# Performance work log

Measured on AMD Instinct MI355X. Metric: run time of the kernel, lower is better.

Reference implementation:

```python
import jax, jax.numpy as jnp
import numpy as np

B, T, IN, HID, OUT, NB = 64, 150, 120, 1024, 35, 8
VTH = 1.0


def _branch_mask(rng, out_dim, in_size):
    # For each output neuron: a random permutation of inputs split into NB equal branches.
    perm = np.argsort(rng.random((out_dim, in_size)), axis=1)          # [out, in]
    branch = (np.arange(in_size) * NB) // in_size                      # branch id of each slot
    rows = (np.arange(out_dim)[:, None] * NB + branch[None, :]).ravel()
    m = np.zeros((out_dim * NB, in_size), dtype=np.bool_)
    m[rows, perm.ravel()] = True
    return jnp.asarray(m)


def setup_inputs() -> dict:
    rng = np.random.default_rng(0)

    def lin(o, i):
        bound = 1.0 / np.sqrt(i)
        w = rng.uniform(-bound, bound, (o, i)).astype(np.float32)
        b = rng.uniform(-bound, bound, (o,)).astype(np.float32)
        return jnp.asarray(w), jnp.asarray(b)

    def tau(*shape):
        return jnp.asarray(rng.uniform(0.0, 4.0, shape).astype(np.float32))

    w1, b1 = lin(HID * NB, IN)
    w2, b2 = lin(HID * NB, HID)
    w3, b3 = lin(HID * NB, HID)
    wr, br = lin(OUT, HID)

    x = jax.random.normal(jax.random.key(0), (B, 1, T, IN), dtype=jnp.float32)

    return dict(
        x=x,
        w1=w1, b1=b1, tau_m1=tau(HID), tau_n1=tau(HID, NB),
        w2=w2, b2=b2, tau_m2=tau(HID), tau_n2=tau(HID, NB),
        w3=w3, b3=b3, tau_m3=tau(HID), tau_n3=tau(HID, NB),
        wr=wr, br=br, tau_mr=tau(OUT),
        mask1=_branch_mask(rng, HID, IN),
        mask2=_branch_mask(rng, HID, HID),
        mask3=_branch_mask(rng, HID, HID),
    )


@jax.custom_vjp
def act_fun(x):  # spike with rectangular surrogate gradient
    return (x > 0.0).astype(x.dtype)

def _act_fwd(x):
    return act_fun(x), x

def _act_bwd(x, g):
    return (g * (jnp.abs(x) < 0.5).astype(g.dtype),)

act_fun.defvjp(_act_fwd, _act_bwd)


def _dh_step(spk_in, d, mem, spk, wm, b, tau_m, tau_n):
    # wm: pre-masked weight [HID*NB, D_in]
    dense = (spk_in @ wm.T + b).reshape(-1, HID, NB)      # [B, HID, NB]
    beta = jax.nn.sigmoid(tau_n)                          # [HID, NB]
    d = beta * d + (1.0 - beta) * dense                   # branch decay
    l_input = d.sum(axis=2)                               # [B, HID]
    alpha = jax.nn.sigmoid(tau_m)
    mem = mem * alpha + (1.0 - alpha) * l_input - VTH * spk  # soft reset (prev spike)
    spk = act_fun(mem - VTH)
    return d, mem, spk


def _forward(x, w1, b1, tau_m1, tau_n1, w2, b2, tau_m2, tau_n2,
             w3, b3, tau_m3, tau_n3, wr, br, tau_mr, mask1, mask2, mask3):
    b_sz = x.shape[0]
    wm1 = w1 * mask1.astype(w1.dtype)
    wm2 = w2 * mask2.astype(w2.dtype)
    wm3 = w3 * mask3.astype(w3.dtype)
    alpha_r = jax.nn.sigmoid(tau_mr)

    xt = x[:, 0].transpose(1, 0, 2)                        # [T, B, IN]

    z_bh = jnp.zeros((b_sz, HID), x.dtype)
    z_bhn = jnp.zeros((b_sz, HID, NB), x.dtype)
    carry0 = (z_bhn, z_bh, z_bh, z_bhn, z_bh, z_bh, z_bhn, z_bh, z_bh,
              jnp.zeros((b_sz, OUT), x.dtype), jnp.zeros((b_sz, OUT), x.dtype))

    def step(carry, inp_t):
        d1, m1, s1, d2, m2, s2, d3, m3, s3, mr, acc = carry
        d1, m1, s1 = _dh_step(inp_t, d1, m1, s1, wm1, b1, tau_m1, tau_n1)
        d2, m2, s2 = _dh_step(s1,    d2, m2, s2, wm2, b2, tau_m2, tau_n2)
        d3, m3, s3 = _dh_step(s2,    d3, m3, s3, wm3, b3, tau_m3, tau_n3)
        mr = mr * alpha_r + (1.0 - alpha_r) * (s3 @ wr.T + br)
        acc = acc + mr
        return (d1, m1, s1, d2, m2, s2, d3, m3, s3, mr, acc), None

    (_, _, _, _, _, _, _, _, _, _, acc), _ = jax.lax.scan(step, carry0, xt)
    return jax.nn.log_softmax(acc / xt.shape[0], axis=1)


def reference(x, w1, b1, tau_m1, tau_n1, w2, b2, tau_m2, tau_n2,
              w3, b3, tau_m3, tau_n3, wr, br, tau_mr, mask1, mask2, mask3):
    return _forward(x, w1, b1, tau_m1, tau_n1, w2, b2, tau_m2, tau_n2,
                    w3, b3, tau_m3, tau_n3, wr, br, tau_mr, mask1, mask2, mask3)
```

## Files before the change

### kernel.cpp

```cpp
#include <hip/hip_runtime.h>
#include <stdint.h>

#define BATCH 64
#define TT    150
#define INSZ  120
#define HID   1024
#define OUTN  35
#define NBR   8
#define TPAD  160
#define CH    8
#define NCHUNK 19

#define XT_OFF  0
#define S1_OFF  4608000
#define S2_OFF  5918720
#define S3_OFF  7229440
#define Y_OFF   8540160
#define ACC_OFF 9884160

__global__ __launch_bounds__(256) void k_tx(const float* __restrict__ x,
                                            float* __restrict__ xT) {
    const int t = blockIdx.x;
    __shared__ float tile[INSZ * 65];
    for (int e = threadIdx.x; e < INSZ * 64; e += 256) {
        const int b = e / INSZ, i = e - b * INSZ;
        tile[i * 65 + b] = x[((size_t)b * TT + t) * INSZ + i];
    }
    __syncthreads();
    for (int e = threadIdx.x; e < INSZ * 64; e += 256) {
        const int i = e >> 6, b = e & 63;
        xT[((size_t)t * INSZ + i) * 64 + b] = tile[i * 65 + b];
    }
}

template <int DIN, int NNZ, int MODE>
__global__ __launch_bounds__(512, 8) void k_layer(
    const float* __restrict__ w,
    const void* __restrict__ maskp,
    const float* __restrict__ bias,
    const float* __restrict__ tau_m,
    const float* __restrict__ tau_n,
    const float* __restrict__ xin,
    const uint64_t* __restrict__ inm,
    uint64_t* __restrict__ outm)
{
    const int tid  = threadIdx.x;
    const int lane = tid & 63;
    const int wid  = tid >> 6;
    const int h    = blockIdx.x;
    const int r    = h * NBR + wid;

    __shared__ uint2 ent[NBR * NNZ];
    __shared__ float red[2][NBR * CH * 64];

    inm = (const uint64_t*)__builtin_assume_aligned(inm, 64);

    const unsigned char* m8  = (const unsigned char*)maskp;
    const int*           m32 = (const int*)maskp;
    {
        const int base = wid * NNZ;
        int cnt = 0;
        for (int c = 0; c * 64 < DIN; ++c) {
            const int i = c * 64 + lane;
            int   mv = 0;
            float wv = 0.f;
            if (i < DIN) {
                mv = m8[(size_t)r * DIN + i];
                wv = w[(size_t)r * DIN + i];
            }
            const unsigned long long bal = __ballot(mv != 0);
            const int pos = __popcll(bal & ((1ull << lane) - 1ull));
            if (mv && cnt + pos < NNZ)
                ent[base + cnt + pos] = make_uint2(__float_as_uint(wv), (unsigned)i);
            cnt += __popcll(bal);
        }
        if (cnt != NNZ) {
            cnt = 0;
            for (int c = 0; c * 64 < DIN; ++c) {
                const int i = c * 64 + lane;
                int   mv = 0;
                float wv = 0.f;
                if (i < DIN) {
                    mv = m32[(size_t)r * DIN + i];
                    wv = w[(size_t)r * DIN + i];
                }
                const unsigned long long bal = __ballot(mv != 0);
                const int pos = __popcll(bal & ((1ull << lane) - 1ull));
                if (mv) ent[base + cnt + pos] =
                            make_uint2(__float_as_uint(wv), (unsigned)i);
                cnt += __popcll(bal);
            }
        }
    }
    __syncthreads();

    const float be = 1.f / (1.f + expf(-tau_n[r]));
    const float om = 1.f - be;
    const float bb = bias[r];
    const float al  = 1.f / (1.f + expf(-tau_m[h]));
    const float oma = 1.f - al;

    float d = 0.f, mem = 0.f, spkprev = 0.f;
    const int base = wid * NNZ;

    for (int tc = 0; tc < NCHUNK; ++tc) {
        const int t0  = tc * CH;
        const int buf = tc & 1;
        float a[CH];
#pragma unroll
        for (int k = 0; k < CH; ++k) a[k] = 0.f;

        if constexpr (MODE == 1) {
#pragma unroll 4
            for (int j = 0; j < NNZ; ++j) {
                const uint2 e  = ent[base + j];
                const int   ix = __builtin_amdgcn_readfirstlane((int)e.y);
                const float wv = __uint_as_float(e.x);
                const ulonglong4* p =
                    (const ulonglong4*)(inm + (size_t)ix * TPAD + t0);
                const ulonglong4 ma = p[0], mb = p[1];
                uint64_t m[CH] = {ma.x, ma.y, ma.z, ma.w,
                                  mb.x, mb.y, mb.z, mb.w};
#pragma unroll
                for (int k = 0; k < CH; ++k) {
                    float s;
                    asm("v_cndmask_b32 %0, 0, %1, %2"
                        : "=v"(s) : "v"(wv), "s"(m[k]));
                    a[k] += s;
                }
            }
        } else {
            const float* xb = xin + (size_t)t0 * DIN * 64;
#pragma unroll 3
            for (int j = 0; j < NNZ; ++j) {
                const uint2 e  = ent[base + j];
                const int   ix = __builtin_amdgcn_readfirstlane((int)e.y);
                const float wv = __uint_as_float(e.x);
#pragma unroll
                for (int k = 0; k < CH; ++k)
                    a[k] += wv * xb[((size_t)k * DIN + ix) * 64 + lane];
            }
        }

#pragma unroll
        for (int k = 0; k < CH; ++k) {
            d = be * d + om * (a[k] + bb);
            red[buf][(wid * CH + k) * 64 + lane] = d;
        }
        __syncthreads();

        if (wid == 0) {
#pragma unroll
            for (int k = 0; k < CH; ++k) {
                const float r0 = red[buf][(0 * CH + k) * 64 + lane];
                const float r1 = red[buf][(1 * CH + k) * 64 + lane];
                const float r2 = red[buf][(2 * CH + k) * 64 + lane];
                const float r3 = red[buf][(3 * CH + k) * 64 + lane];
                const float r4 = red[buf][(4 * CH + k) * 64 + lane];
                const float r5 = red[buf][(5 * CH + k) * 64 + lane];
                const float r6 = red[buf][(6 * CH + k) * 64 + lane];
                const float r7 = red[buf][(7 * CH + k) * 64 + lane];
                const float p01 = r0 + r1, p23 = r2 + r3;
                const float p45 = r4 + r5, p67 = r6 + r7;
                const float l = ((p01 + p23) + p45) + p67;
                if (t0 + k < TT) {
                    mem = al * mem + oma * l - spkprev;
                    spkprev = (mem > 1.0f) ? 1.f : 0.f;
                    const unsigned long long bal = __ballot(mem > 1.0f);
                    if (lane == 0) outm[(size_t)h * TPAD + (t0 + k)] = bal;
                }
            }
        }
    }
}

__global__ __launch_bounds__(256) void k_ry(const float* __restrict__ wr,
                                            const uint64_t* __restrict__ s3m,
                                            float* __restrict__ Y) {
    const int lane  = threadIdx.x & 63;
    const int wid   = __builtin_amdgcn_readfirstlane(threadIdx.x >> 6);
    const int o  = blockIdx.x / NCHUNK;
    const int t0 = (blockIdx.x % NCHUNK) * CH;
    s3m = (const uint64_t*)__builtin_assume_aligned(s3m, 64);
    const float* wrow = wr + (size_t)o * HID;
    __shared__ float red[4 * CH * 64];
    float acc[CH];
#pragma unroll
    for (int k = 0; k < CH; ++k) acc[k] = 0.f;
#pragma unroll 4
    for (int ii = 0; ii < HID / 4; ++ii) {
        const int i = wid * (HID / 4) + ii;
        const float wv = wrow[i];
        const ulonglong4* p =
            (const ulonglong4*)(s3m + (size_t)i * TPAD + t0);
        const ulonglong4 ma = p[0], mb = p[1];
        uint64_t m[CH] = {ma.x, ma.y, ma.z, ma.w, mb.x, mb.y, mb.z, mb.w};
#pragma unroll
        for (int k = 0; k < CH; ++k) {
            float s;
            asm("v_cndmask_b32 %0, 0, %1, %2" : "=v"(s) : "v"(wv), "s"(m[k]));
            acc[k] += s;
        }
    }
#pragma unroll
    for (int k = 0; k < CH; ++k)
        red[(wid * CH + k) * 64 + lane] = acc[k];
    __syncthreads();
    if (wid == 0) {
#pragma unroll
        for (int k = 0; k < CH; ++k) {
            if (t0 + k >= TT) break;
            const float v = ((red[(0 * CH + k) * 64 + lane]
                            + red[(1 * CH + k) * 64 + lane])
                            + red[(2 * CH + k) * 64 + lane])
                            + red[(3 * CH + k) * 64 + lane];
            Y[((size_t)(t0 + k) * OUTN + o) * 64 + lane] = v;
        }
    }
}

__global__ void k_racc(const float* __restrict__ Y,
                       const float* __restrict__ br,
                       const float* __restrict__ tau_mr,
                       float* __restrict__ ACC) {
    const int o = blockIdx.x, lane = threadIdx.x;
    const float ar  = 1.f / (1.f + expf(-tau_mr[o]));
    const float bro = br[o];
    float acc = 0.f, q = ar;
    for (int t = TT - 1; t >= 0; --t) {
        const float y = Y[((size_t)t * OUTN + o) * 64 + lane] + bro;
        acc += y * (1.f - q);
        q *= ar;
    }
    ACC[o * 64 + lane] = acc;
}

__global__ void k_smax(const float* __restrict__ ACC, float* __restrict__ out) {
    const int b = threadIdx.x;
    float v[OUTN];
    float mx = -3.4e38f;
    for (int o = 0; o < OUTN; ++o) {
        v[o] = ACC[o * 64 + b] / (float)TT;
        mx = fmaxf(mx, v[o]);
    }
    float sum = 0.f;
    for (int o = 0; o < OUTN; ++o) sum += expf(v[o] - mx);
    const float lse = mx + logf(sum);
    for (int o = 0; o < OUTN; ++o) out[b * OUTN + o] = v[o] - lse;
}

extern "C" void kernel_launch(void* const* d_in, const int* in_sizes, int n_in,
                              void* d_out, int out_size, void* d_ws,
                              size_t ws_size, hipStream_t stream) {
    (void)in_sizes; (void)n_in; (void)out_size; (void)ws_size;
    const float* x   = (const float*)d_in[0];
    const float* w1  = (const float*)d_in[1];
    const float* b1  = (const float*)d_in[2];
    const float* tm1 = (const float*)d_in[3];
    const float* tn1 = (const float*)d_in[4];
    const float* w2  = (const float*)d_in[5];
    const float* b2  = (const float*)d_in[6];
    const float* tm2 = (const float*)d_in[7];
    const float* tn2 = (const float*)d_in[8];
    const float* w3  = (const float*)d_in[9];
    const float* b3  = (const float*)d_in[10];
    const float* tm3 = (const float*)d_in[11];
    const float* tn3 = (const float*)d_in[12];
    const float* wr  = (const float*)d_in[13];
    const float* br  = (const float*)d_in[14];
    const float* tmr = (const float*)d_in[15];
    const void*  m1  = d_in[16];
    const void*  m2  = d_in[17];
    const void*  m3  = d_in[18];
    float* out = (float*)d_out;

    char* ws = (char*)d_ws;
    float*    xT  = (float*)(ws + XT_OFF);
    uint64_t* s1m = (uint64_t*)(ws + S1_OFF);
    uint64_t* s2m = (uint64_t*)(ws + S2_OFF);
    uint64_t* s3m = (uint64_t*)(ws + S3_OFF);
    float*    Y   = (float*)(ws + Y_OFF);
    float*    ACC = (float*)(ws + ACC_OFF);

    k_tx<<<TT, 256, 0, stream>>>(x, xT);
    k_layer<INSZ, 15, 0><<<HID, 512, 0, stream>>>(
        w1, m1, b1, tm1, tn1, xT, nullptr, s1m);
    k_layer<HID, 128, 1><<<HID, 512, 0, stream>>>(
        w2, m2, b2, tm2, tn2, nullptr, s1m, s2m);
    k_layer<HID, 128, 1><<<HID, 512, 0, stream>>>(
        w3, m3, b3, tm3, tn3, nullptr, s2m, s3m);
    k_ry<<<OUTN * NCHUNK, 256, 0, stream>>>(wr, s3m, Y);
    k_racc<<<OUTN, 64, 0, stream>>>(Y, br, tmr, ACC);
    k_smax<<<1, 64, 0, stream>>>(ACC, out);
}
```

Before: 1.657 ms.

## Pre-pack sparse weights into compact global arrays and relayout input transpose

```diff
diff --git a/kernel.cpp b/kernel.cpp
--- a/kernel.cpp
+++ b/kernel.cpp
@@ -1,42 +1,79 @@
 #include <hip/hip_runtime.h>
 #include <stdint.h>
 
-#define BATCH 64
-#define TT    150
-#define INSZ  120
-#define HID   1024
-#define OUTN  35
-#define NBR   8
-#define TPAD  160
-#define CH    8
+#define TT     150
+#define INSZ   120
+#define HID    1024
+#define OUTN   35
+#define NBR    8
+#define TP     152
+#define CH     8
 #define NCHUNK 19
 
-#define XT_OFF  0
-#define S1_OFF  4608000
-#define S2_OFF  5918720
-#define S3_OFF  7229440
-#define Y_OFF   8540160
-#define ACC_OFF 9884160
-
-__global__ __launch_bounds__(256) void k_tx(const float* __restrict__ x,
-                                            float* __restrict__ xT) {
-    const int t = blockIdx.x;
-    __shared__ float tile[INSZ * 65];
-    for (int e = threadIdx.x; e < INSZ * 64; e += 256) {
-        const int b = e / INSZ, i = e - b * INSZ;
-        tile[i * 65 + b] = x[((size_t)b * TT + t) * INSZ + i];
-    }
-    __syncthreads();
-    for (int e = threadIdx.x; e < INSZ * 64; e += 256) {
-        const int i = e >> 6, b = e & 63;
-        xT[((size_t)t * INSZ + i) * 64 + b] = tile[i * 65 + b];
-    }
-}
-
-template <int DIN, int NNZ, int MODE>
+#define SA_OFF   0
+#define SB_OFF   1245184
+#define PK_OFF   2490368
+#define XT_OFF   3538944
+#define Y_OFF    2490368
+#define ACC_OFF  3866624
+
+template <int DIN, int NNZ_EXPECT, int NNZ_OUT, int RSTRIDE, int WOFF>
+__global__ __launch_bounds__(512) void k_pack(
+    const float* __restrict__ w, const void* __restrict__ maskp,
+    uint8_t* __restrict__ dst) {
+    const int lane = threadIdx.x & 63;
+    const int wid  = __builtin_amdgcn_readfirstlane(threadIdx.x >> 6);
+    const int r    = blockIdx.x * 8 + wid;
+    uint16_t* di = (uint16_t*)(dst + (size_t)r * RSTRIDE);
+    float*    dw = (float*)(dst + (size_t)r * RSTRIDE + WOFF);
+    const unsigned char* m8  = (const unsigned char*)maskp;
+    const int*           m32 = (const int*)maskp;
+
+    int cnt = 0;
+    for (int c = 0; c * 64 < DIN; ++c) {
+        const int i = c * 64 + lane;
+        int   mv = 0; float wv = 0.f;
+        if (i < DIN) { mv = m8[(size_t)r * DIN + i]; wv = w[(size_t)r * DIN + i]; }
+        const unsigned long long bal = __ballot(mv != 0);
+        const int pos = __popcll(bal & ((1ull << lane) - 1ull));
+        if (mv && cnt + pos < NNZ_OUT) { di[cnt + pos] = (uint16_t)i; dw[cnt + pos] = wv; }
+        cnt += __popcll(bal);
+    }
+    if (cnt != NNZ_EXPECT) {
+        cnt = 0;
+        for (int c = 0; c * 64 < DIN; ++c) {
+            const int i = c * 64 + lane;
+            int   mv = 0; float wv = 0.f;
+            if (i < DIN) { mv = m32[(size_t)r * DIN + i]; wv = w[(size_t)r * DIN + i]; }
+            const unsigned long long bal = __ballot(mv != 0);
+            const int pos = __popcll(bal & ((1ull << lane) - 1ull));
+            if (mv && cnt + pos < NNZ_OUT) { di[cnt + pos] = (uint16_t)i; dw[cnt + pos] = wv; }
+            cnt += __popcll(bal);
+        }
+    }
+    for (int f = cnt + lane; f < NNZ_OUT; f += 64) { di[f] = 0; dw[f] = 0.f; }
+}
+
+__global__ __launch_bounds__(256) void k_tx2(const float* __restrict__ x,
+                                             float* __restrict__ xT2) {
+    const int e = blockIdx.x * 256 + threadIdx.x;
+    const int c = e / 7680;
+    const int rem = e - c * 7680;
+    const int b = rem / INSZ, i = rem - b * INSZ;
+    float v[CH];
+#pragma unroll
+    for (int k = 0; k < CH; ++k) {
+        const int t = c * CH + k;
+        v[k] = (t < TT) ? x[((size_t)b * TT + t) * INSZ + i] : 0.f;
+    }
+    float* dst = xT2 + ((size_t)i * 64 + b) * TP + c * CH;
+    *(float4*)dst       = make_float4(v[0], v[1], v[2], v[3]);
+    *(float4*)(dst + 4) = make_float4(v[4], v[5], v[6], v[7]);
+}
+
+template <int DIN, int NNZ, int MODE, int RSTRIDE, int WOFF>
 __global__ __launch_bounds__(512, 8) void k_layer(
-    const float* __restrict__ w,
-    const void* __restrict__ maskp,
+    const uint8_t* __restrict__ pk,
     const float* __restrict__ bias,
     const float* __restrict__ tau_m,
     const float* __restrict__ tau_n,
@@ -44,55 +81,17 @@
     const uint64_t* __restrict__ inm,
     uint64_t* __restrict__ outm)
 {
-    const int tid  = threadIdx.x;
-    const int lane = tid & 63;
-    const int wid  = tid >> 6;
+    const int lane = threadIdx.x & 63;
+    const int wid  = __builtin_amdgcn_readfirstlane(threadIdx.x >> 6);
     const int h    = blockIdx.x;
     const int r    = h * NBR + wid;
 
-    __shared__ uint2 ent[NBR * NNZ];
     __shared__ float red[2][NBR * CH * 64];
 
+    const uint8_t*  pkrow = pk + (size_t)r * RSTRIDE;
+    const uint32_t* idxp  = (const uint32_t*)pkrow;
+    const float*    wp    = (const float*)(pkrow + WOFF);
     inm = (const uint64_t*)__builtin_assume_aligned(inm, 64);
-
-    const unsigned char* m8  = (const unsigned char*)maskp;
-    const int*           m32 = (const int*)maskp;
-    {
-        const int base = wid * NNZ;
-        int cnt = 0;
-        for (int c = 0; c * 64 < DIN; ++c) {
-            const int i = c * 64 + lane;
-            int   mv = 0;
-            float wv = 0.f;
-            if (i < DIN) {
-                mv = m8[(size_t)r * DIN + i];
-                wv = w[(size_t)r * DIN + i];
-            }
-            const unsigned long long bal = __ballot(mv != 0);
-            const int pos = __popcll(bal & ((1ull << lane) - 1ull));
-            if (mv && cnt + pos < NNZ)
-                ent[base + cnt + pos] = make_uint2(__float_as_uint(wv), (unsigned)i);
-            cnt += __popcll(bal);
-        }
-        if (cnt != NNZ) {
-            cnt = 0;
-            for (int c = 0; c * 64 < DIN; ++c) {
-                const int i = c * 64 + lane;
-                int   mv = 0;
-                float wv = 0.f;
-                if (i < DIN) {
-                    mv = m32[(size_t)r * DIN + i];
-                    wv = w[(size_t)r * DIN + i];
-                }
-                const unsigned long long bal = __ballot(mv != 0);
-                const int pos = __popcll(bal & ((1ull << lane) - 1ull));
-                if (mv) ent[base + cnt + pos] =
-                            make_uint2(__float_as_uint(wv), (unsigned)i);
-                cnt += __popcll(bal);
-            }
-        }
-    }
-    __syncthreads();
 
     const float be = 1.f / (1.f + expf(-tau_n[r]));
     const float om = 1.f - be;
@@ -101,7 +100,6 @@
     const float oma = 1.f - al;
 
     float d = 0.f, mem = 0.f, spkprev = 0.f;
-    const int base = wid * NNZ;
 
     for (int tc = 0; tc < NCHUNK; ++tc) {
         const int t0  = tc * CH;
@@ -111,34 +109,54 @@
         for (int k = 0; k < CH; ++k) a[k] = 0.f;
 
         if constexpr (MODE == 1) {
-#pragma unroll 4
-            for (int j = 0; j < NNZ; ++j) {
-                const uint2 e  = ent[base + j];
-                const int   ix = __builtin_amdgcn_readfirstlane((int)e.y);
-                const float wv = __uint_as_float(e.x);
-                const ulonglong4* p =
-                    (const ulonglong4*)(inm + (size_t)ix * TPAD + t0);
-                const ulonglong4 ma = p[0], mb = p[1];
-                uint64_t m[CH] = {ma.x, ma.y, ma.z, ma.w,
-                                  mb.x, mb.y, mb.z, mb.w};
+            for (int jj = 0; jj < NNZ / 2; ++jj) {
+                const uint32_t pair = idxp[jj];
+                const int ix0 = (int)(pair & 0xffffu);
+                const int ix1 = (int)(pair >> 16);
+                const float2 wpair = ((const float2*)wp)[jj];
+                const float w0 = wpair.x, w1 = wpair.y;
+                const ulonglong4* p0 =
+                    (const ulonglong4*)(inm + (size_t)ix0 * TP + t0);
+                const ulonglong4* p1 =
+                    (const ulonglong4*)(inm + (size_t)ix1 * TP + t0);
+                const ulonglong4 a0 = p0[0], b0 = p0[1];
+                const ulonglong4 a1 = p1[0], b1 = p1[1];
+                const uint64_t m0[CH] = {a0.x, a0.y, a0.z, a0.w,
+                                         b0.x, b0.y, b0.z, b0.w};
+                const uint64_t m1[CH] = {a1.x, a1.y, a1.z, a1.w,
+                                         b1.x, b1.y, b1.z, b1.w};
 #pragma unroll
                 for (int k = 0; k < CH; ++k) {
-                    float s;
+                    float s0, s1;
                     asm("v_cndmask_b32 %0, 0, %1, %2"
-                        : "=v"(s) : "v"(wv), "s"(m[k]));
-                    a[k] += s;
+                        : "=v"(s0) : "v"(w0), "s"(m0[k]));
+                    a[k] += s0;
+                    asm("v_cndmask_b32 %0, 0, %1, %2"
+                        : "=v"(s1) : "v"(w1), "s"(m1[k]));
+                    a[k] += s1;
                 }
             }
         } else {
-            const float* xb = xin + (size_t)t0 * DIN * 64;
-#pragma unroll 3
-            for (int j = 0; j < NNZ; ++j) {
-                const uint2 e  = ent[base + j];
-                const int   ix = __builtin_amdgcn_readfirstlane((int)e.y);
-                const float wv = __uint_as_float(e.x);
-#pragma unroll
-                for (int k = 0; k < CH; ++k)
-                    a[k] += wv * xb[((size_t)k * DIN + ix) * 64 + lane];
+            for (int jj = 0; jj < NNZ / 2; ++jj) {
+                const uint32_t pair = idxp[jj];
+                const int ix0 = (int)(pair & 0xffffu);
+                const int ix1 = (int)(pair >> 16);
+                const float2 wpair = ((const float2*)wp)[jj];
+                const float w0 = wpair.x, w1 = wpair.y;
+                const float* q0 = xin + (size_t)ix0 * (64 * TP) + lane * TP + t0;
+                const float* q1 = xin + (size_t)ix1 * (64 * TP) + lane * TP + t0;
+                const float4 xa0 = *(const float4*)q0;
+                const float4 xb0 = *(const float4*)(q0 + 4);
+                const float4 xa1 = *(const float4*)q1;
+                const float4 xb1 = *(const float4*)(q1 + 4);
+                a[0] += w0 * xa0.x; a[1] += w0 * xa0.y;
+                a[2] += w0 * xa0.z; a[3] += w0 * xa0.w;
+                a[4] += w0 * xb0.x; a[5] += w0 * xb0.y;
+                a[6] += w0 * xb0.z; a[7] += w0 * xb0.w;
+                a[0] += w1 * xa1.x; a[1] += w1 * xa1.y;
+                a[2] += w1 * xa1.z; a[3] += w1 * xa1.w;
+                a[4] += w1 * xb1.x; a[5] += w1 * xb1.y;
+                a[6] += w1 * xb1.z; a[7] += w1 * xb1.w;
             }
         }
 
@@ -167,7 +185,7 @@
                     mem = al * mem + oma * l - spkprev;
                     spkprev = (mem > 1.0f) ? 1.f : 0.f;
                     const unsigned long long bal = __ballot(mem > 1.0f);
-                    if (lane == 0) outm[(size_t)h * TPAD + (t0 + k)] = bal;
+                    if (lane == 0) outm[(size_t)h * TP + (t0 + k)] = bal;
                 }
             }
         }
@@ -191,10 +209,9 @@
     for (int ii = 0; ii < HID / 4; ++ii) {
         const int i = wid * (HID / 4) + ii;
         const float wv = wrow[i];
-        const ulonglong4* p =
-            (const ulonglong4*)(s3m + (size_t)i * TPAD + t0);
+        const ulonglong4* p = (const ulonglong4*)(s3m + (size_t)i * TP + t0);
         const ulonglong4 ma = p[0], mb = p[1];
-        uint64_t m[CH] = {ma.x, ma.y, ma.z, ma.w, mb.x, mb.y, mb.z, mb.w};
+        const uint64_t m[CH] = {ma.x, ma.y, ma.z, ma.w, mb.x, mb.y, mb.z, mb.w};
 #pragma unroll
         for (int k = 0; k < CH; ++k) {
             float s;
@@ -275,21 +292,24 @@
     float* out = (float*)d_out;
 
     char* ws = (char*)d_ws;
-    float*    xT  = (float*)(ws + XT_OFF);
-    uint64_t* s1m = (uint64_t*)(ws + S1_OFF);
-    uint64_t* s2m = (uint64_t*)(ws + S2_OFF);
-    uint64_t* s3m = (uint64_t*)(ws + S3_OFF);
+    uint64_t* sA  = (uint64_t*)(ws + SA_OFF);
+    uint64_t* sB  = (uint64_t*)(ws + SB_OFF);
+    uint8_t*  PK  = (uint8_t*)(ws + PK_OFF);
+    float*    xT2 = (float*)(ws + XT_OFF);
     float*    Y   = (float*)(ws + Y_OFF);
     float*    ACC = (float*)(ws + ACC_OFF);
 
-    k_tx<<<TT, 256, 0, stream>>>(x, xT);
-    k_layer<INSZ, 15, 0><<<HID, 512, 0, stream>>>(
-        w1, m1, b1, tm1, tn1, xT, nullptr, s1m);
-    k_layer<HID, 128, 1><<<HID, 512, 0, stream>>>(
-        w2, m2, b2, tm2, tn2, nullptr, s1m, s2m);
-    k_layer<HID, 128, 1><<<HID, 512, 0, stream>>>(
-        w3, m3, b3, tm3, tn3, nullptr, s2m, s3m);
-    k_ry<<<OUTN * NCHUNK, 256, 0, stream>>>(wr, s3m, Y);
+    k_pack<INSZ, 15, 16, 128, 32><<<HID, 512, 0, stream>>>(w1, m1, PK);
+    k_tx2<<<570, 256, 0, stream>>>(x, xT2);
+    k_layer<INSZ, 16, 0, 128, 32><<<HID, 512, 0, stream>>>(
+        PK, b1, tm1, tn1, xT2, nullptr, sA);
+    k_pack<HID, 128, 128, 768, 256><<<HID, 512, 0, stream>>>(w2, m2, PK);
+    k_layer<HID, 128, 1, 768, 256><<<HID, 512, 0, stream>>>(
+        PK, b2, tm2, tn2, nullptr, sA, sB);
+    k_pack<HID, 128, 128, 768, 256><<<HID, 512, 0, stream>>>(w3, m3, PK);
+    k_layer<HID, 128, 1, 768, 256><<<HID, 512, 0, stream>>>(
+        PK, b3, tm3, tn3, nullptr, sB, sA);
+    k_ry<<<OUTN * NCHUNK, 256, 0, stream>>>(wr, sA, Y);
     k_racc<<<OUTN, 64, 0, stream>>>(Y, br, tmr, ACC);
     k_smax<<<1, 64, 0, stream>>>(ACC, out);
 }
```

Measured after the change: 2.430 ms. 1.47x slower.
